# Performance work log

Measured on AMD Instinct MI355X. Metric: run time of the kernel, lower is better.

The kernel has to match this reference:

```python
import jax, jax.numpy as jnp
import numpy as np

N, D, C = 2048, 192, 100000
S, M = 30.0, 0.2

def setup_inputs() -> dict:
    key = jax.random.key(0)
    k1, k2, k3 = jax.random.split(key, 3)
    x = jax.random.normal(k1, (N, D), dtype=jnp.float32)
    W = jax.random.normal(k2, (C, D), dtype=jnp.float32) * 0.05
    label = jax.random.randint(k3, (N,), 0, C, dtype=jnp.int64)
    return {"x": x, "W": W, "label": label}

def reference(x, W, label):
    # NOTE: the original torch code's weight-normalization loop is a no-op
    # (it rebinds the local name W, never mutating the parameter), so W is
    # intentionally NOT normalized here; only x is.
    xn = x / jnp.linalg.norm(x, axis=1, keepdims=True)          # [N, D]
    wf = jnp.einsum("nd,cd->nc", xn, W)                          # [N, C]
    tgt = jnp.take_along_axis(wf, label[:, None], axis=1)[:, 0]  # [N]
    numer = S * (tgt - M)                                        # margin-adjusted target logit
    logits = S * wf
    # replace the label column with the margin-adjusted numerator so that
    # logsumexp(logits) == log(exp(numer) + sum_{j!=y} exp(s*wf[:,j]))
    logits = logits.at[jnp.arange(N), label].set(numer)
    L = numer - jax.nn.logsumexp(logits, axis=1)                 # [N]
    return -jnp.mean(L)
```

## Files before the change

kernel.cpp:

```cpp
#include <hip/hip_runtime.h>
#include <stdint.h>


constexpr int N  = 2048;
constexpr int D  = 192;
constexpr int C  = 100000;
constexpr int KT = D / 32;
constexpr int TILE = 512;
constexpr int RT16 = C / 16;
constexpr int TPG = 12;
constexpr int CX = 523;
constexpr int NT16 = CX * TPG;
constexpr float PHANTOM = (float)(NT16 * 16 - C);
constexpr int BANDS = 4;
constexpr int RYB = N / (64 * BANDS);
constexpr int BUF = 4 * KT * TILE;
constexpr int NXB = N / 4;

#define S_SCALE 30.0f
#define MARGIN  0.2f
#define S_LOG2E 43.2808512266689f

using short8 = __attribute__((ext_vector_type(8))) short;
using f32x4  = __attribute__((ext_vector_type(4))) float;

typedef __attribute__((address_space(1))) const void GV;
typedef __attribute__((address_space(3))) void LV;

__device__ inline unsigned short f2bf(float f) {
  unsigned int u = __float_as_uint(f);
  u += 0x7fffu + ((u >> 16) & 1u);
  return (unsigned short)(u >> 16);
}

__device__ inline int pack_idx(int r, int k) {
  return ((r >> 4) * KT + (k >> 5)) * TILE + (((k >> 3) & 3) * 16 + (r & 15)) * 8 + (k & 7);
}

__device__ inline float row_sum16(float v) {
  int x;
  x = __float_as_int(v);
  v += __int_as_float(__builtin_amdgcn_update_dpp(0, x, 0x128, 0xF, 0xF, true));
  x = __float_as_int(v);
  v += __int_as_float(__builtin_amdgcn_update_dpp(0, x, 0x124, 0xF, 0xF, true));
  x = __float_as_int(v);
  v += __int_as_float(__builtin_amdgcn_update_dpp(0, x, 0x04E, 0xF, 0xF, true));
  x = __float_as_int(v);
  v += __int_as_float(__builtin_amdgcn_update_dpp(0, x, 0x0B1, 0xF, 0xF, true));
  return v;
}

__global__ __launch_bounds__(256) void prep_all(
    const float* __restrict__ x, const float* __restrict__ W,
    unsigned short* __restrict__ xnb, unsigned short* __restrict__ Wb,
    float* __restrict__ out) {
  const int bid  = blockIdx.x;
  const int lane = threadIdx.x & 63;
  if (bid == 0 && threadIdx.x == 0) out[0] = 0.0f;

  if (bid < NXB) {
    const int row = bid * 4 + (threadIdx.x >> 6);
    const float* xr = x + (size_t)row * D;
    float v0 = xr[lane], v1 = xr[lane + 64], v2 = xr[lane + 128];
    float ss = v0 * v0 + v1 * v1 + v2 * v2;
#pragma unroll
    for (int off = 32; off > 0; off >>= 1) ss += __shfl_xor(ss, off, 64);
    const float inv = rsqrtf(ss) * S_LOG2E;
    xnb[pack_idx(row, lane)]       = f2bf(v0 * inv);
    xnb[pack_idx(row, lane + 64)]  = f2bf(v1 * inv);
    xnb[pack_idx(row, lane + 128)] = f2bf(v2 * inv);
  } else {
    const int t16 = (bid - NXB) * 4 + (threadIdx.x >> 6);
    const int m = lane & 15, q = lane >> 4;
    unsigned short* dst = Wb + (size_t)t16 * KT * TILE + lane * 8;
    if (t16 < RT16) {
      const float* src = W + (size_t)(t16 * 16 + m) * D + q * 8;
#pragma unroll
      for (int ks = 0; ks < KT; ++ks) {
        const float4* s4 = (const float4*)(src + ks * 32);
        float4 f0 = s4[0], f1 = s4[1];
        short8 hv;
        hv[0] = (short)f2bf(f0.x); hv[1] = (short)f2bf(f0.y);
        hv[2] = (short)f2bf(f0.z); hv[3] = (short)f2bf(f0.w);
        hv[4] = (short)f2bf(f1.x); hv[5] = (short)f2bf(f1.y);
        hv[6] = (short)f2bf(f1.z); hv[7] = (short)f2bf(f1.w);
        *(short8*)(dst + (size_t)ks * TILE) = hv;
      }
    } else {
      const short8 z = {0, 0, 0, 0, 0, 0, 0, 0};
#pragma unroll
      for (int ks = 0; ks < KT; ++ks) *(short8*)(dst + (size_t)ks * TILE) = z;
    }
  }
}

__global__ __launch_bounds__(256, 3) void gemm_lse(
    const unsigned short* __restrict__ xnb,
    const unsigned short* __restrict__ Wb,
    float* __restrict__ partial) {
  __shared__ alignas(16) unsigned short As[2 * BUF];
  __shared__ alignas(16) float rs_lds[4][256];

  const int tid = threadIdx.x;
  const int bid = blockIdx.x;
  const int cx = bid >> 3, ry = bid & 7;

  {
    const unsigned short* slab = xnb + (size_t)(ry * BANDS) * BUF;
#pragma unroll
    for (int i = 0; i < 6; ++i) {
      const int chunk = tid + i * 256;
      __builtin_amdgcn_global_load_lds(
          (GV*)((const char*)slab + (size_t)chunk * 16),
          (LV*)((char*)As + (size_t)chunk * 16), 16, 0, 0);
    }
  }

  const int lane = tid & 63, wave = tid >> 6;
  const int m = lane & 15, quad = lane >> 4;

  short8 breg[3][KT];
#pragma unroll
  for (int tc = 0; tc < 3; ++tc)
#pragma unroll
    for (int ks = 0; ks < KT; ++ks)
      breg[tc][ks] = *(const short8*)(
          Wb + (size_t)((cx * TPG + wave * 3 + tc) * KT + ks) * TILE + lane * 8);

  const f32x4 zero4 = {0.0f, 0.0f, 0.0f, 0.0f};

  for (int b = 0; b < BANDS; ++b) {
    __syncthreads();

    if (b + 1 < BANDS) {
      const unsigned short* slab = xnb + (size_t)(ry * BANDS + b + 1) * BUF;
      char* dst = (char*)&As[((b + 1) & 1) * BUF];
#pragma unroll
      for (int i = 0; i < 6; ++i) {
        const int chunk = tid + i * 256;
        __builtin_amdgcn_global_load_lds(
            (GV*)((const char*)slab + (size_t)chunk * 16),
            (LV*)(dst + (size_t)chunk * 16), 16, 0, 0);
      }
    }

    const unsigned short* Ab = &As[(b & 1) * BUF];

    f32x4 acc[4][3];
#pragma unroll
    for (int a = 0; a < 4; ++a)
#pragma unroll
      for (int c = 0; c < 3; ++c) acc[a][c] = zero4;

#pragma unroll
    for (int ks = 0; ks < KT; ++ks) {
      short8 af[4];
#pragma unroll
      for (int tr = 0; tr < 4; ++tr)
        af[tr] = *(const short8*)(&Ab[(tr * KT + ks) * TILE + lane * 8]);
#pragma unroll
      for (int tr = 0; tr < 4; ++tr)
#pragma unroll
        for (int tc = 0; tc < 3; ++tc)
          acc[tr][tc] = __builtin_amdgcn_mfma_f32_16x16x32_bf16(
              af[tr], breg[tc][ks], acc[tr][tc], 0, 0, 0);
    }

#pragma unroll
    for (int tr = 0; tr < 4; ++tr) {
      float rv0 = 0.f, rv1 = 0.f, rv2 = 0.f, rv3 = 0.f;
#pragma unroll
      for (int tc = 0; tc < 3; ++tc) {
        rv0 += __builtin_amdgcn_exp2f(acc[tr][tc][0]);
        rv1 += __builtin_amdgcn_exp2f(acc[tr][tc][1]);
        rv2 += __builtin_amdgcn_exp2f(acc[tr][tc][2]);
        rv3 += __builtin_amdgcn_exp2f(acc[tr][tc][3]);
      }
      rv0 = row_sum16(rv0);
      rv1 = row_sum16(rv1);
      rv2 = row_sum16(rv2);
      rv3 = row_sum16(rv3);
      if (m == 0) {
        float4 v = make_float4(rv0, rv1, rv2, rv3);
        *(float4*)(&rs_lds[wave][b * 64 + tr * 16 + quad * 4]) = v;
      }
    }
  }

  __syncthreads();
  if (tid < 256) {
    const float s = rs_lds[0][tid] + rs_lds[1][tid] + rs_lds[2][tid] + rs_lds[3][tid];
    partial[(size_t)cx * N + ry * 256 + tid] = s;
  }
}

__global__ __launch_bounds__(256) void finalize_rows(
    const float* __restrict__ x, const float* __restrict__ W,
    const int* __restrict__ label, const float* __restrict__ partial,
    float* __restrict__ out) {
  const int row  = blockIdx.x * 4 + (threadIdx.x >> 6);
  const int lane = threadIdx.x & 63;
  const float* xr = x + (size_t)row * D;
  float v0 = xr[lane], v1 = xr[lane + 64], v2 = xr[lane + 128];
  float ss = v0 * v0 + v1 * v1 + v2 * v2;
  const int lab = label[row];
  const float* wr = W + (size_t)lab * D;
  float d = v0 * wr[lane] + v1 * wr[lane + 64] + v2 * wr[lane + 128];
  float p = 0.0f;
  for (int s = lane; s < CX; s += 64) p += partial[(size_t)s * N + row];
#pragma unroll
  for (int off = 32; off > 0; off >>= 1) {
    ss += __shfl_xor(ss, off, 64);
    d  += __shfl_xor(d,  off, 64);
    p  += __shfl_xor(p,  off, 64);
  }
  __shared__ float part[4];
  if (lane == 0) {
    const float tgt   = d * rsqrtf(ss);
    const float numer = S_SCALE * (tgt - MARGIN);
    const float se = p - PHANTOM - __expf(S_SCALE * tgt) + __expf(numer);
    part[threadIdx.x >> 6] = numer - logf(se);
  }
  __syncthreads();
  if (threadIdx.x == 0) {
    const float blocksum = part[0] + part[1] + part[2] + part[3];
    atomicAdd(out, -blocksum * (1.0f / (float)N));
  }
}

extern "C" void kernel_launch(void* const* d_in, const int* in_sizes, int n_in,
                              void* d_out, int out_size, void* d_ws, size_t ws_size,
                              hipStream_t stream) {
  const float* x     = (const float*)d_in[0];
  const float* W     = (const float*)d_in[1];
  const int*   label = (const int*)d_in[2];
  float*       out   = (float*)d_out;

  char* ws = (char*)d_ws;
  size_t off = 0;
  unsigned short* xnb = (unsigned short*)(ws + off); off += (size_t)N * D * 2;
  unsigned short* Wb  = (unsigned short*)(ws + off); off += (size_t)NT16 * KT * TILE * 2;
  float* partial = (float*)(ws + off); off += (size_t)CX * N * 4;

  prep_all<<<NXB + NT16 / 4, 256, 0, stream>>>(x, W, xnb, Wb, out);

  gemm_lse<<<CX * RYB, 256, 0, stream>>>(xnb, Wb, partial);

  finalize_rows<<<N / 4, 256, 0, stream>>>(x, W, label, partial, out);
}
```

Baseline: 212.0 us.

## Fuse W bf16 conversion into GEMM kernel and drop packed W workspace

Removes the W-packing pass from the prep kernel. Each GEMM block now loads its fp32 W tiles straight into registers and converts them to bf16 there, which avoids writing and re-reading a packed bf16 copy of W. The grid is remapped so column tiles vary fastest, with a padded column count and early-exit blocks, and the phantom-column correction is adjusted. The cost is that every row band re-reads fp32 W, which is twice as many bytes per read. The new block order also spreads the eight readers of a W tile far apart in launch order, which may reduce cache reuse.

```diff
diff --git a/kernel.cpp b/kernel.cpp
--- a/kernel.cpp
+++ b/kernel.cpp
@@ -9,13 +9,12 @@
 constexpr int TILE = 512;
 constexpr int RT16 = C / 16;
 constexpr int TPG = 12;
-constexpr int CX = 523;
-constexpr int NT16 = CX * TPG;
-constexpr float PHANTOM = (float)(NT16 * 16 - C);
+constexpr int CX = 521;
+constexpr int CXP = 528;
+constexpr float PHANTOM = (float)(CX * TPG * 16 - C);
 constexpr int BANDS = 4;
 constexpr int RYB = N / (64 * BANDS);
 constexpr int BUF = 4 * KT * TILE;
-constexpr int NXB = N / 4;
 
 #define S_SCALE 30.0f
 #define MARGIN  0.2f
@@ -50,31 +49,55 @@
   return v;
 }
 
-__global__ __launch_bounds__(256) void prep_all(
-    const float* __restrict__ x, const float* __restrict__ W,
-    unsigned short* __restrict__ xnb, unsigned short* __restrict__ Wb,
-    float* __restrict__ out) {
-  const int bid  = blockIdx.x;
+__global__ __launch_bounds__(256) void prep_x(const float* __restrict__ x,
+                                              unsigned short* __restrict__ xnb,
+                                              float* __restrict__ out) {
+  if (blockIdx.x == 0 && threadIdx.x == 0) out[0] = 0.0f;
+  const int row  = blockIdx.x * 4 + (threadIdx.x >> 6);
   const int lane = threadIdx.x & 63;
-  if (bid == 0 && threadIdx.x == 0) out[0] = 0.0f;
-
-  if (bid < NXB) {
-    const int row = bid * 4 + (threadIdx.x >> 6);
-    const float* xr = x + (size_t)row * D;
-    float v0 = xr[lane], v1 = xr[lane + 64], v2 = xr[lane + 128];
-    float ss = v0 * v0 + v1 * v1 + v2 * v2;
-#pragma unroll
-    for (int off = 32; off > 0; off >>= 1) ss += __shfl_xor(ss, off, 64);
-    const float inv = rsqrtf(ss) * S_LOG2E;
-    xnb[pack_idx(row, lane)]       = f2bf(v0 * inv);
-    xnb[pack_idx(row, lane + 64)]  = f2bf(v1 * inv);
-    xnb[pack_idx(row, lane + 128)] = f2bf(v2 * inv);
-  } else {
-    const int t16 = (bid - NXB) * 4 + (threadIdx.x >> 6);
-    const int m = lane & 15, q = lane >> 4;
-    unsigned short* dst = Wb + (size_t)t16 * KT * TILE + lane * 8;
-    if (t16 < RT16) {
-      const float* src = W + (size_t)(t16 * 16 + m) * D + q * 8;
+  const float* xr = x + (size_t)row * D;
+  float v0 = xr[lane], v1 = xr[lane + 64], v2 = xr[lane + 128];
+  float ss = v0 * v0 + v1 * v1 + v2 * v2;
+#pragma unroll
+  for (int off = 32; off > 0; off >>= 1) ss += __shfl_xor(ss, off, 64);
+  const float inv = rsqrtf(ss) * S_LOG2E;
+  xnb[pack_idx(row, lane)]       = f2bf(v0 * inv);
+  xnb[pack_idx(row, lane + 64)]  = f2bf(v1 * inv);
+  xnb[pack_idx(row, lane + 128)] = f2bf(v2 * inv);
+}
+
+__global__ __launch_bounds__(256, 3) void gemm_lse(
+    const unsigned short* __restrict__ xnb,
+    const float* __restrict__ Wf,
+    float* __restrict__ partial) {
+  __shared__ alignas(16) unsigned short As[2 * BUF];
+  __shared__ alignas(16) float rs_lds[4][256];
+
+  const int tid = threadIdx.x;
+  const int bid = blockIdx.x;
+  const int cx = bid % CXP, ry = bid / CXP;
+  if (cx >= CX) return;
+
+  {
+    const unsigned short* slab = xnb + (size_t)(ry * BANDS) * BUF;
+#pragma unroll
+    for (int i = 0; i < 6; ++i) {
+      const int chunk = tid + i * 256;
+      __builtin_amdgcn_global_load_lds(
+          (GV*)((const char*)slab + (size_t)chunk * 16),
+          (LV*)((char*)As + (size_t)chunk * 16), 16, 0, 0);
+    }
+  }
+
+  const int lane = tid & 63, wave = tid >> 6;
+  const int m = lane & 15, quad = lane >> 4;
+
+  short8 breg[3][KT];
+#pragma unroll
+  for (int tc = 0; tc < 3; ++tc) {
+    const int gt = cx * TPG + wave * 3 + tc;
+    if (gt < RT16) {
+      const float* src = Wf + (size_t)(gt * 16 + m) * D + quad * 8;
 #pragma unroll
       for (int ks = 0; ks < KT; ++ks) {
         const float4* s4 = (const float4*)(src + ks * 32);
@@ -84,48 +107,14 @@
         hv[2] = (short)f2bf(f0.z); hv[3] = (short)f2bf(f0.w);
         hv[4] = (short)f2bf(f1.x); hv[5] = (short)f2bf(f1.y);
         hv[6] = (short)f2bf(f1.z); hv[7] = (short)f2bf(f1.w);
-        *(short8*)(dst + (size_t)ks * TILE) = hv;
+        breg[tc][ks] = hv;
       }
     } else {
       const short8 z = {0, 0, 0, 0, 0, 0, 0, 0};
 #pragma unroll
-      for (int ks = 0; ks < KT; ++ks) *(short8*)(dst + (size_t)ks * TILE) = z;
-    }
-  }
-}
-
-__global__ __launch_bounds__(256, 3) void gemm_lse(
-    const unsigned short* __restrict__ xnb,
-    const unsigned short* __restrict__ Wb,
-    float* __restrict__ partial) {
-  __shared__ alignas(16) unsigned short As[2 * BUF];
-  __shared__ alignas(16) float rs_lds[4][256];
-
-  const int tid = threadIdx.x;
-  const int bid = blockIdx.x;
-  const int cx = bid >> 3, ry = bid & 7;
-
-  {
-    const unsigned short* slab = xnb + (size_t)(ry * BANDS) * BUF;
-#pragma unroll
-    for (int i = 0; i < 6; ++i) {
-      const int chunk = tid + i * 256;
-      __builtin_amdgcn_global_load_lds(
-          (GV*)((const char*)slab + (size_t)chunk * 16),
-          (LV*)((char*)As + (size_t)chunk * 16), 16, 0, 0);
-    }
-  }
-
-  const int lane = tid & 63, wave = tid >> 6;
-  const int m = lane & 15, quad = lane >> 4;
-
-  short8 breg[3][KT];
-#pragma unroll
-  for (int tc = 0; tc < 3; ++tc)
-#pragma unroll
-    for (int ks = 0; ks < KT; ++ks)
-      breg[tc][ks] = *(const short8*)(
-          Wb + (size_t)((cx * TPG + wave * 3 + tc) * KT + ks) * TILE + lane * 8);
+      for (int ks = 0; ks < KT; ++ks) breg[tc][ks] = z;
+    }
+  }
 
   const f32x4 zero4 = {0.0f, 0.0f, 0.0f, 0.0f};
 
@@ -239,12 +228,11 @@
   char* ws = (char*)d_ws;
   size_t off = 0;
   unsigned short* xnb = (unsigned short*)(ws + off); off += (size_t)N * D * 2;
-  unsigned short* Wb  = (unsigned short*)(ws + off); off += (size_t)NT16 * KT * TILE * 2;
   float* partial = (float*)(ws + off); off += (size_t)CX * N * 4;
 
-  prep_all<<<NXB + NT16 / 4, 256, 0, stream>>>(x, W, xnb, Wb, out);
-
-  gemm_lse<<<CX * RYB, 256, 0, stream>>>(xnb, Wb, partial);
+  prep_x<<<N / 4, 256, 0, stream>>>(x, xnb, out);
+
+  gemm_lse<<<CXP * RYB, 256, 0, stream>>>(xnb, W, partial);
 
   finalize_rows<<<N / 4, 256, 0, stream>>>(x, W, label, partial, out);
 }
```

New measurement: 237.5 us. 12.1% more time.
